# Kernel tuning notes

Hardware: AMD Instinct MI355X
Metric: run time of the kernel (lower is better)

## Reference

```python
import jax, jax.numpy as jnp
import numpy as np
from functools import partial

NPOINT = 1024
RADIUS = 0.2
NSAMPLE = 32
IN_CH = 64
MLP = [64, 64, 128]
EPS = 1e-5
B, N = 8, 4096


def setup_inputs() -> dict:
    key = jax.random.key(0)
    ks = jax.random.split(key, 2 + 2 * len(MLP))
    inp = {
        "xyz": jax.random.uniform(ks[0], (B, N, 3), jnp.float32),
        "points": jax.random.normal(ks[1], (B, N, IN_CH), jnp.float32),
    }
    last = IN_CH + 3
    for i, out in enumerate(MLP):
        # Conv2d 1x1 weight (out, in), kaiming-ish scale; BN gamma=1, beta=0
        inp[f"w{i}"] = jax.random.normal(ks[2 + 2 * i], (out, last), jnp.float32) / np.float32(np.sqrt(last))
        inp[f"b{i}"] = jnp.zeros((out,), jnp.float32)
        inp[f"g{i}"] = jnp.ones((out,), jnp.float32)
        inp[f"bt{i}"] = jnp.zeros((out,), jnp.float32)
        last = out
    return inp


def farthest_point_sample(xyz, npoint):
    # xyz: (B,N,3) -> (B,npoint) int32. Deterministic start at index 0
    # (original torch code uses randint for the seed point).
    Bb, Nn, _ = xyz.shape

    def step(carry, _):
        distance, farthest = carry
        centroid = jnp.take_along_axis(xyz, farthest[:, None, None], axis=1)  # (B,1,3)
        dist = jnp.sum((xyz - centroid) ** 2, axis=-1)                         # (B,N)
        distance = jnp.minimum(distance, dist)
        nxt = jnp.argmax(distance, axis=-1).astype(jnp.int32)
        return (distance, nxt), farthest

    init = (jnp.full((Bb, Nn), 1e10, xyz.dtype), jnp.zeros((Bb,), jnp.int32))
    _, idx = jax.lax.scan(step, init, None, length=npoint)  # (npoint,B)
    return idx.T


def query_ball_point(radius, nsample, xyz, new_xyz):
    # xyz: (B,N,3), new_xyz: (B,S,3) -> (B,S,nsample) indices into N
    Nn = xyz.shape[1]
    # (B,S,N) squared distances -- the big memory-bound intermediate
    sqrdists = jnp.sum((new_xyz[:, :, None, :] - xyz[:, None, :, :]) ** 2, axis=-1)
    group_idx = jnp.where(sqrdists > radius ** 2, Nn, jnp.arange(Nn, dtype=jnp.int32))
    group_idx = jnp.sort(group_idx, axis=-1)[:, :, :nsample]
    first = group_idx[:, :, :1]
    return jnp.where(group_idx == Nn, first, group_idx)


def _gather(p, i):
    # p: (N,C), i: (...,) -> (..., C)
    return p[i]


index_points = jax.vmap(_gather)  # batched over B


def reference(xyz, points, w0, b0, g0, bt0, w1, b1, g1, bt1, w2, b2, g2, bt2):
    fps_idx = farthest_point_sample(xyz, NPOINT)                # (B,S)
    new_xyz = index_points(xyz, fps_idx)                        # (B,S,3)
    group_idx = query_ball_point(RADIUS, NSAMPLE, xyz, new_xyz)  # (B,S,K)
    grouped_xyz = index_points(xyz, group_idx) - new_xyz[:, :, None, :]  # (B,S,K,3)
    grouped_pts = index_points(points, group_idx)               # (B,S,K,D)
    x = jnp.concatenate([grouped_xyz, grouped_pts], axis=-1)    # (B,S,K,3+D)

    for w, b, g, bt in ((w0, b0, g0, bt0), (w1, b1, g1, bt1), (w2, b2, g2, bt2)):
        x = jnp.einsum('bskc,oc->bsko', x, w) + b               # 1x1 conv
        mu = jnp.mean(x, axis=(0, 1, 2))                        # BN (training-mode batch stats)
        var = jnp.var(x, axis=(0, 1, 2))
        x = jax.nn.relu(g * (x - mu) * jax.lax.rsqrt(var + EPS) + bt)

    new_points = jnp.max(x, axis=2)                             # max over neighbors K -> (B,S,C')
    return new_xyz, new_points
```

## Files before the change

### kernel.cpp

```cpp
#include <hip/hip_runtime.h>
#include <cmath>

#define NB 8
#define NPTS 4096
#define NPT 1024
#define NSAMP 32
#define MTOT (NB*NPT*NSAMP)
#define NBLK 4096

typedef float v2f __attribute__((ext_vector_type(2)));

__global__ __launch_bounds__(512) void fps_kernel(const float* __restrict__ xyz,
                                                  float* __restrict__ new_xyz) {
#pragma clang fp contract(off)
  const int b = blockIdx.x;
  const int t = threadIdx.x;
  const int wv = t >> 6;
  const int lane = t & 63;
  __shared__ float4 sxyz[NPTS];
  __shared__ float4 sout[NPT];
  __shared__ unsigned long long skey[2][8];
  const float* X = xyz + (size_t)b * NPTS * 3;
  v2f px[4], py[4], pz[4], dist[4];
#pragma unroll
  for (int i = 0; i < 4; ++i) {
    int p0 = (2 * i) * 512 + t;
    int p1 = (2 * i + 1) * 512 + t;
    float x0 = X[p0 * 3 + 0], y0 = X[p0 * 3 + 1], z0 = X[p0 * 3 + 2];
    float x1 = X[p1 * 3 + 0], y1 = X[p1 * 3 + 1], z1 = X[p1 * 3 + 2];
    px[i] = (v2f){x0, x1}; py[i] = (v2f){y0, y1}; pz[i] = (v2f){z0, z1};
    sxyz[p0] = make_float4(x0, y0, z0, 0.0f);
    sxyz[p1] = make_float4(x1, y1, z1, 0.0f);
    dist[i] = (v2f){1e10f, 1e10f};
  }
  __syncthreads();
  float ccx = X[0], ccy = X[1], ccz = X[2];
  for (int s = 0; s < NPT; ++s) {
    if (t == 0) sout[s] = make_float4(ccx, ccy, ccz, 0.0f);
    v2f cx = (v2f){ccx, ccx}, cy = (v2f){ccy, ccy}, cz = (v2f){ccz, ccz};
    v2f nd[4];
#pragma unroll
    for (int i = 0; i < 4; ++i) {
      v2f dx = px[i] - cx;
      v2f dy = py[i] - cy;
      v2f dz = pz[i] - cz;
      v2f d = (dx * dx + dy * dy) + dz * dz;
      v2f m = __builtin_elementwise_min(dist[i], d);
      dist[i] = m;
      nd[i] = m;
    }
    v2f t01 = __builtin_elementwise_max(nd[0], nd[1]);
    v2f t23 = __builtin_elementwise_max(nd[2], nd[3]);
    v2f t03 = __builtin_elementwise_max(t01, t23);
    float lmax = fmaxf(t03.x, t03.y);
    unsigned km = __float_as_uint(lmax);
    {
      unsigned o;
      o = (unsigned)__builtin_amdgcn_update_dpp(0, (int)km, 0x111, 0xf, 0xf, false);
      km = o > km ? o : km;
      o = (unsigned)__builtin_amdgcn_update_dpp(0, (int)km, 0x112, 0xf, 0xf, false);
      km = o > km ? o : km;
      o = (unsigned)__builtin_amdgcn_update_dpp(0, (int)km, 0x114, 0xf, 0xf, false);
      km = o > km ? o : km;
      o = (unsigned)__builtin_amdgcn_update_dpp(0, (int)km, 0x118, 0xf, 0xf, false);
      km = o > km ? o : km;
      o = (unsigned)__builtin_amdgcn_update_dpp(0, (int)km, 0x142, 0xf, 0xf, false);
      km = o > km ? o : km;
      o = (unsigned)__builtin_amdgcn_update_dpp(0, (int)km, 0x143, 0xf, 0xf, false);
      km = o > km ? o : km;
    }
    unsigned wmax = (unsigned)__builtin_amdgcn_readlane((int)km, 63);
    unsigned long long m0 = __ballot(__float_as_uint(nd[0].x) == wmax);
    unsigned long long m1 = __ballot(__float_as_uint(nd[0].y) == wmax);
    unsigned long long m2 = __ballot(__float_as_uint(nd[1].x) == wmax);
    unsigned long long m3 = __ballot(__float_as_uint(nd[1].y) == wmax);
    unsigned long long m4 = __ballot(__float_as_uint(nd[2].x) == wmax);
    unsigned long long m5 = __ballot(__float_as_uint(nd[2].y) == wmax);
    unsigned long long m6 = __ballot(__float_as_uint(nd[3].x) == wmax);
    unsigned long long m7 = __ballot(__float_as_uint(nd[3].y) == wmax);
    unsigned long long mk = m7; int ord = 7;
    if (m6) { mk = m6; ord = 6; }
    if (m5) { mk = m5; ord = 5; }
    if (m4) { mk = m4; ord = 4; }
    if (m3) { mk = m3; ord = 3; }
    if (m2) { mk = m2; ord = 2; }
    if (m1) { mk = m1; ord = 1; }
    if (m0) { mk = m0; ord = 0; }
    int wlane = (int)__builtin_ctzll(mk);
    int idx = ord * 512 + wv * 64 + wlane;
    unsigned long long key = ((unsigned long long)wmax << 32)
                           | (unsigned int)(~idx);
    int par = s & 1;
    if (lane == 0) skey[par][wv] = key;
    __syncthreads();
    const ulonglong2* sk = (const ulonglong2*)skey[par];
    ulonglong2 A = sk[0], B = sk[1], C = sk[2], D = sk[3];
    unsigned long long a = A.x > A.y ? A.x : A.y;
    unsigned long long bq = B.x > B.y ? B.x : B.y;
    unsigned long long c = C.x > C.y ? C.x : C.y;
    unsigned long long dq = D.x > D.y ? D.x : D.y;
    unsigned long long ab = a > bq ? a : bq;
    unsigned long long cd = c > dq ? c : dq;
    unsigned long long kf = ab > cd ? ab : cd;
    int far = (int)(~(unsigned int)kf) & (NPTS - 1);
    float4 cc = sxyz[far];
    ccx = cc.x; ccy = cc.y; ccz = cc.z;
  }
  __syncthreads();
  float* outp = new_xyz + (size_t)b * NPT * 3;
  for (int j = t; j < NPT; j += 512) {
    float4 c = sout[j];
    outp[3 * j + 0] = c.x; outp[3 * j + 1] = c.y; outp[3 * j + 2] = c.z;
  }
}

__global__ __launch_bounds__(256) void ballq_kernel(const float* __restrict__ xyz,
                                                    const float* __restrict__ new_xyz,
                                                    int* __restrict__ gidx) {
  int w = (blockIdx.x * 256 + threadIdx.x) >> 6;
  int lane = threadIdx.x & 63;
  int b = w >> 10;
  const float* X = xyz + (size_t)b * NPTS * 3;
  float cx = new_xyz[w * 3 + 0], cy = new_xyz[w * 3 + 1], cz = new_xyz[w * 3 + 2];
  int* out = gidx + (size_t)w * NSAMP;
  int cnt = 0, first = -1;
  for (int c = 0; c < NPTS / 64; ++c) {
    int p = c * 64 + lane;
    float dx = __fsub_rn(X[p * 3 + 0], cx);
    float dy = __fsub_rn(X[p * 3 + 1], cy);
    float dz = __fsub_rn(X[p * 3 + 2], cz);
    float d = __fadd_rn(__fadd_rn(__fmul_rn(dx, dx), __fmul_rn(dy, dy)), __fmul_rn(dz, dz));
    bool inr = !(d > 0.04f);
    unsigned long long mask = __ballot(inr);
    if (mask) {
      if (first < 0) first = c * 64 + (int)__builtin_ctzll(mask);
      if (inr) {
        int pos = cnt + (int)__builtin_popcountll(mask & ((1ull << lane) - 1ull));
        if (pos < NSAMP) out[pos] = p;
      }
      cnt += (int)__builtin_popcountll(mask);
      if (cnt >= NSAMP) break;
    }
  }
  if (lane >= cnt && lane < NSAMP) out[lane] = first;
}

__global__ __launch_bounds__(256) void mlp_gemm_gather(
    const float* __restrict__ xyz, const float* __restrict__ points,
    const float* __restrict__ new_xyz, const int* __restrict__ gidx,
    const float* __restrict__ Wg, const float* __restrict__ bias,
    float* __restrict__ Yg, float* __restrict__ partials) {
  constexpr int O = 64, OJ = 4, KP4 = 17;
  __shared__ __align__(16) float sX[64 * 68];
  __shared__ __align__(16) float sWt[68 * O];
  const int t = threadIdx.x;
  const int m0 = blockIdx.x * 64;

  for (int i = t; i < O * 68; i += 256) {
    int k = i >> 6, o = i & 63;
    float w;
    if (k < 64) w = Wg[o * 67 + k + 3];
    else if (k < 67) w = Wg[o * 67 + (k - 64)];
    else w = 0.0f;
    sWt[k * O + o] = w;
  }
  {
    int r = t >> 2, q = t & 3;
    int m = m0 + r;
    int idx = gidx[m];
    int b = m >> 15;
    const float* prow = points + ((size_t)b * NPTS + idx) * 64;
#pragma unroll
    for (int c4 = q; c4 < 16; c4 += 4)
      *(float4*)&sX[r * 68 + 4 * c4] = *(const float4*)(prow + 4 * c4);
    if (q == 0) {
      int g = m >> 5;
      const float* xr = xyz + ((size_t)b * NPTS + idx) * 3;
      sX[r * 68 + 64] = __fsub_rn(xr[0], new_xyz[g * 3 + 0]);
      sX[r * 68 + 65] = __fsub_rn(xr[1], new_xyz[g * 3 + 1]);
      sX[r * 68 + 66] = __fsub_rn(xr[2], new_xyz[g * 3 + 2]);
      sX[r * 68 + 67] = 0.0f;
    }
  }
  __syncthreads();

  const int to = t & 15, tm = t >> 4;
  float acc[4][OJ];
#pragma unroll
  for (int i = 0; i < 4; ++i)
#pragma unroll
    for (int j = 0; j < OJ; ++j) acc[i][j] = 0.0f;

#pragma unroll
  for (int k4 = 0; k4 < KP4; ++k4) {
    float xs[4][4];
#pragma unroll
    for (int i = 0; i < 4; ++i) {
      float4 v = *(const float4*)&sX[(4 * tm + i) * 68 + 4 * k4];
      xs[i][0] = v.x; xs[i][1] = v.y; xs[i][2] = v.z; xs[i][3] = v.w;
    }
#pragma unroll
    for (int kk = 0; kk < 4; ++kk) {
      float4 wq = *(const float4*)&sWt[(4 * k4 + kk) * O + OJ * to];
      float wv[4] = {wq.x, wq.y, wq.z, wq.w};
#pragma unroll
      for (int i = 0; i < 4; ++i) {
        float xv = xs[i][kk];
#pragma unroll
        for (int j = 0; j < OJ; ++j) acc[i][j] = fmaf(xv, wv[j], acc[i][j]);
      }
    }
  }
#pragma unroll
  for (int j = 0; j < OJ; ++j) {
    float bb = bias[OJ * to + j];
#pragma unroll
    for (int i = 0; i < 4; ++i) acc[i][j] += bb;
  }
  float ps[OJ], ss[OJ];
#pragma unroll
  for (int j = 0; j < OJ; ++j) {
    ps[j] = ((acc[0][j] + acc[1][j]) + (acc[2][j] + acc[3][j]));
    ss[j] = ((acc[0][j] * acc[0][j] + acc[1][j] * acc[1][j]) +
             (acc[2][j] * acc[2][j] + acc[3][j] * acc[3][j]));
  }
  __syncthreads();
#pragma unroll
  for (int j = 0; j < OJ; ++j) {
    int o = OJ * to + j;
    sX[tm * O + o] = ps[j];
    sX[16 * O + tm * O + o] = ss[j];
  }
  __syncthreads();
  if (t < O) {
    float s1 = 0.0f, s2 = 0.0f;
#pragma unroll
    for (int r2 = 0; r2 < 16; ++r2) { s1 += sX[r2 * O + t]; s2 += sX[16 * O + r2 * O + t]; }
    partials[(size_t)t * NBLK + blockIdx.x] = s1;
    partials[(size_t)(O + t) * NBLK + blockIdx.x] = s2;
  }
#pragma unroll
  for (int i = 0; i < 4; ++i)
    *(float4*)&Yg[(size_t)(m0 + 4 * tm + i) * O + OJ * to] =
        make_float4(acc[i][0], acc[i][1], acc[i][2], acc[i][3]);
}

template<int O, bool WRITE_Y, bool DO_MM>
__global__ __launch_bounds__(256) void mlp_gemm(const float* __restrict__ Xg,
                                                const float* __restrict__ Wg,
                                                const float* __restrict__ bias,
                                                const float* __restrict__ ad,
                                                float* __restrict__ Yg,
                                                float* __restrict__ partials,
                                                float* __restrict__ mm) {
  constexpr int KDIM = 64, KP4 = 16;
  constexpr int OJ = O / 16;
  __shared__ __align__(16) float sX[64 * 68];
  __shared__ __align__(16) float sWt[KDIM * O];
  const int t = threadIdx.x;
  const int m0 = blockIdx.x * 64;

  for (int i = t; i < O * KDIM; i += 256) {
    int k = i / O;
    int o = i - k * O;
    sWt[k * O + o] = Wg[o * KDIM + k];
  }
  {
    int r = t >> 2, q = t & 3;
    const float* src = Xg + (size_t)(m0 + r) * KDIM;
    for (int c4 = q; c4 < KP4; c4 += 4) {
      float4 v = *(const float4*)(src + 4 * c4);
      float4 a = *(const float4*)(ad + 4 * c4);
      float4 d = *(const float4*)(ad + 128 + 4 * c4);
      v.x = fmaxf(fmaf(a.x, v.x, d.x), 0.0f);
      v.y = fmaxf(fmaf(a.y, v.y, d.y), 0.0f);
      v.z = fmaxf(fmaf(a.z, v.z, d.z), 0.0f);
      v.w = fmaxf(fmaf(a.w, v.w, d.w), 0.0f);
      *(float4*)&sX[r * 68 + 4 * c4] = v;
    }
  }
  __syncthreads();

  const int to = t & 15, tm = t >> 4;
  float acc[4][OJ];
#pragma unroll
  for (int i = 0; i < 4; ++i)
#pragma unroll
    for (int j = 0; j < OJ; ++j) acc[i][j] = 0.0f;

#pragma unroll
  for (int k4 = 0; k4 < KP4; ++k4) {
    float xs[4][4];
#pragma unroll
    for (int i = 0; i < 4; ++i) {
      float4 v = *(const float4*)&sX[(4 * tm + i) * 68 + 4 * k4];
      xs[i][0] = v.x; xs[i][1] = v.y; xs[i][2] = v.z; xs[i][3] = v.w;
    }
#pragma unroll
    for (int kk = 0; kk < 4; ++kk) {
      float wv[OJ];
#pragma unroll
      for (int j4 = 0; j4 < OJ / 4; ++j4) {
        float4 wq = *(const float4*)&sWt[(4 * k4 + kk) * O + OJ * to + 4 * j4];
        wv[4 * j4 + 0] = wq.x; wv[4 * j4 + 1] = wq.y;
        wv[4 * j4 + 2] = wq.z; wv[4 * j4 + 3] = wq.w;
      }
#pragma unroll
      for (int i = 0; i < 4; ++i) {
        float xv = xs[i][kk];
#pragma unroll
        for (int j = 0; j < OJ; ++j) acc[i][j] = fmaf(xv, wv[j], acc[i][j]);
      }
    }
  }
#pragma unroll
  for (int j = 0; j < OJ; ++j) {
    float bb = bias[OJ * to + j];
#pragma unroll
    for (int i = 0; i < 4; ++i) acc[i][j] += bb;
  }
  float ps[OJ], ss[OJ];
#pragma unroll
  for (int j = 0; j < OJ; ++j) {
    ps[j] = ((acc[0][j] + acc[1][j]) + (acc[2][j] + acc[3][j]));
    ss[j] = ((acc[0][j] * acc[0][j] + acc[1][j] * acc[1][j]) +
             (acc[2][j] * acc[2][j] + acc[3][j] * acc[3][j]));
  }
  __syncthreads();
#pragma unroll
  for (int j = 0; j < OJ; ++j) {
    int o = OJ * to + j;
    sX[tm * O + o] = ps[j];
    sX[16 * O + tm * O + o] = ss[j];
  }
  __syncthreads();
  if (t < O) {
    float s1 = 0.0f, s2 = 0.0f;
#pragma unroll
    for (int r2 = 0; r2 < 16; ++r2) { s1 += sX[r2 * O + t]; s2 += sX[16 * O + r2 * O + t]; }
    partials[(size_t)t * NBLK + blockIdx.x] = s1;
    partials[(size_t)(O + t) * NBLK + blockIdx.x] = s2;
  }
  if constexpr (WRITE_Y) {
#pragma unroll
    for (int i = 0; i < 4; ++i) {
#pragma unroll
      for (int j4 = 0; j4 < OJ / 4; ++j4) {
        *(float4*)&Yg[(size_t)(m0 + 4 * tm + i) * O + OJ * to + 4 * j4] =
            make_float4(acc[i][4 * j4 + 0], acc[i][4 * j4 + 1],
                        acc[i][4 * j4 + 2], acc[i][4 * j4 + 3]);
      }
    }
  }
  if constexpr (DO_MM) {
    float vmx[OJ], vmn[OJ];
#pragma unroll
    for (int j = 0; j < OJ; ++j) {
      vmx[j] = fmaxf(fmaxf(acc[0][j], acc[1][j]), fmaxf(acc[2][j], acc[3][j]));
      vmn[j] = fminf(fminf(acc[0][j], acc[1][j]), fminf(acc[2][j], acc[3][j]));
    }
    __syncthreads();
#pragma unroll
    for (int j = 0; j < OJ; ++j) {
      int o = OJ * to + j;
      sX[tm * O + o] = vmx[j];
      sX[16 * O + tm * O + o] = vmn[j];
    }
    __syncthreads();
    int g = t >> 7, o = t & 127;
    float mx = sX[(g * 8) * O + o];
    float mn = sX[16 * O + (g * 8) * O + o];
#pragma unroll
    for (int r2 = 1; r2 < 8; ++r2) {
      mx = fmaxf(mx, sX[(g * 8 + r2) * O + o]);
      mn = fminf(mn, sX[16 * O + (g * 8 + r2) * O + o]);
    }
    int row = (m0 >> 5) + g;
    mm[(size_t)row * O + o] = mx;
    mm[(size_t)8192 * O + (size_t)row * O + o] = mn;
  }
}

__global__ __launch_bounds__(256) void bn_finalize(const float* __restrict__ partials,
                                                   const float* __restrict__ g,
                                                   const float* __restrict__ bt,
                                                   float* __restrict__ ad, int O) {
  int o = blockIdx.x, t = threadIdx.x;
  const float* p1 = partials + (size_t)o * NBLK;
  const float* p2 = partials + (size_t)(O + o) * NBLK;
  float s1 = 0.0f, s2 = 0.0f;
  for (int i = t; i < NBLK; i += 256) { s1 += p1[i]; s2 += p2[i]; }
  __shared__ float r1[4], r2[4];
#pragma unroll
  for (int off = 32; off >= 1; off >>= 1) {
    s1 += __shfl_down(s1, off, 64);
    s2 += __shfl_down(s2, off, 64);
  }
  if ((t & 63) == 0) { r1[t >> 6] = s1; r2[t >> 6] = s2; }
  __syncthreads();
  if (t == 0) {
    float S1 = (r1[0] + r1[1]) + (r1[2] + r1[3]);
    float S2 = (r2[0] + r2[1]) + (r2[2] + r2[3]);
    const float invM = 1.0f / (float)MTOT;
    float mu = S1 * invM;
    float var = S2 * invM - mu * mu;
    float rs = 1.0f / sqrtf(var + 1e-5f);
    float a = g[o] * rs;
    ad[o] = a;
    ad[128 + o] = bt[o] - mu * a;
  }
}

__global__ __launch_bounds__(256) void final_kernel(const float* __restrict__ mm,
                                                    const float* __restrict__ ad,
                                                    float* __restrict__ out) {
  int gid = blockIdx.x * 256 + threadIdx.x;
  int o = gid & 127;
  float a = ad[o], d = ad[128 + o];
  float y = (a >= 0.0f) ? mm[gid] : mm[8192 * 128 + gid];
  out[gid] = fmaxf(fmaf(a, y, d), 0.0f);
}

extern "C" void kernel_launch(void* const* d_in, const int* in_sizes, int n_in,
                              void* d_out, int out_size, void* d_ws, size_t ws_size,
                              hipStream_t stream) {
  (void)in_sizes; (void)n_in; (void)out_size; (void)ws_size;
  const float* xyz    = (const float*)d_in[0];
  const float* points = (const float*)d_in[1];
  const float* w0  = (const float*)d_in[2];
  const float* b0  = (const float*)d_in[3];
  const float* g0  = (const float*)d_in[4];
  const float* bt0 = (const float*)d_in[5];
  const float* w1  = (const float*)d_in[6];
  const float* b1  = (const float*)d_in[7];
  const float* g1  = (const float*)d_in[8];
  const float* bt1 = (const float*)d_in[9];
  const float* w2  = (const float*)d_in[10];
  const float* b2  = (const float*)d_in[11];
  const float* g2  = (const float*)d_in[12];
  const float* bt2 = (const float*)d_in[13];

  float* out      = (float*)d_out;
  float* new_xyz  = out;
  float* out_pts  = out + 24576;

  float* wsf  = (float*)d_ws;
  int*   gidx = (int*)d_ws;
  float* Y2   = wsf + 262144;
  float* Y1   = Y2 + (size_t)MTOT * 68;
  float* part = Y1 + (size_t)MTOT * 64;
  float* ad1  = part + 2 * 128 * NBLK;
  float* ad2  = ad1 + 256;
  float* ad3  = ad2 + 256;
  float* mm   = ad3 + 256;

  fps_kernel<<<NB, 512, 0, stream>>>(xyz, new_xyz);
  ballq_kernel<<<(NB * NPT * 64) / 256, 256, 0, stream>>>(xyz, new_xyz, gidx);

  mlp_gemm_gather<<<NBLK, 256, 0, stream>>>(xyz, points, new_xyz, gidx,
                                            w0, b0, Y1, part);
  bn_finalize<<<64, 256, 0, stream>>>(part, g0, bt0, ad1, 64);

  mlp_gemm<64, true, false><<<NBLK, 256, 0, stream>>>(
      Y1, w1, b1, ad1, Y2, part, nullptr);
  bn_finalize<<<64, 256, 0, stream>>>(part, g1, bt1, ad2, 64);

  mlp_gemm<128, false, true><<<NBLK, 256, 0, stream>>>(
      Y2, w2, b2, ad2, nullptr, part, mm);
  bn_finalize<<<128, 256, 0, stream>>>(part, g2, bt2, ad3, 128);

  final_kernel<<<(8192 * 128) / 256, 256, 0, stream>>>(mm, ad3, out_pts);
}
```

Baseline: 920.0 us.

## Replace FP32 SIMT MLP GEMMs with FP16 MFMA matrix-core kernels

The three 1x1-conv GEMM kernels now run on 16x16x32 f16 MFMA instructions instead of scalar FP32 FMAs. Activations are packed to half precision when staged into shared memory, and a new prep kernel pre-transposes and converts the weights to padded fp16 layouts. The BN partial-sum and min/max reductions are reworked around the MFMA output layout using wave shuffles. This trades FP32 inputs for fp16 ones, which may hurt accuracy in the batch-norm statistics.

New measurement: 794.0 us. -13.7%, faster.

```diff
diff --git a/kernel.cpp b/kernel.cpp
--- a/kernel.cpp
+++ b/kernel.cpp
@@ -9,6 +9,41 @@
 #define NBLK 4096
 
 typedef float v2f __attribute__((ext_vector_type(2)));
+typedef _Float16 half8 __attribute__((ext_vector_type(8)));
+typedef float f32x4 __attribute__((ext_vector_type(4)));
+
+__device__ __forceinline__ unsigned int pk2h(float a, float b) {
+  _Float16 ha = (_Float16)a, hb = (_Float16)b;
+  unsigned short ua = __builtin_bit_cast(unsigned short, ha);
+  unsigned short ub = __builtin_bit_cast(unsigned short, hb);
+  return (unsigned int)ua | ((unsigned int)ub << 16);
+}
+__device__ __forceinline__ unsigned short f2h(float v) {
+  _Float16 h = (_Float16)v;
+  return __builtin_bit_cast(unsigned short, h);
+}
+
+__global__ __launch_bounds__(256) void prep_weights(
+    const float* __restrict__ w0, const float* __restrict__ w1,
+    const float* __restrict__ w2, unsigned short* __restrict__ Wt1,
+    unsigned short* __restrict__ Wt2, unsigned short* __restrict__ Wt3) {
+  int i = blockIdx.x * 256 + threadIdx.x;
+  if (i < 64 * 104) {
+    int o = i / 104, k = i - o * 104;
+    float v = 0.0f;
+    if (k < 64) v = w0[o * 67 + k + 3];
+    else if (k < 67) v = w0[o * 67 + (k - 64)];
+    Wt1[i] = f2h(v);
+  } else if (i < 64 * 104 + 64 * 72) {
+    int j = i - 64 * 104;
+    int o = j / 72, k = j - o * 72;
+    Wt2[j] = (k < 64) ? f2h(w1[o * 64 + k]) : (unsigned short)0;
+  } else if (i < 64 * 104 + 64 * 72 + 128 * 72) {
+    int l = i - 64 * 104 - 64 * 72;
+    int o = l / 72, k = l - o * 72;
+    Wt3[l] = (k < 64) ? f2h(w2[o * 64 + k]) : (unsigned short)0;
+  }
+}
 
 __global__ __launch_bounds__(512) void fps_kernel(const float* __restrict__ xyz,
                                                   float* __restrict__ new_xyz) {
@@ -145,239 +180,171 @@
   if (lane >= cnt && lane < NSAMP) out[lane] = first;
 }
 
-__global__ __launch_bounds__(256) void mlp_gemm_gather(
-    const float* __restrict__ xyz, const float* __restrict__ points,
-    const float* __restrict__ new_xyz, const int* __restrict__ gidx,
-    const float* __restrict__ Wg, const float* __restrict__ bias,
-    float* __restrict__ Yg, float* __restrict__ partials) {
-  constexpr int O = 64, OJ = 4, KP4 = 17;
-  __shared__ __align__(16) float sX[64 * 68];
-  __shared__ __align__(16) float sWt[68 * O];
+template<int KB, int KS, int O, bool GATHER, bool NORM_IN, bool WRITE_Y, bool DO_MM>
+__global__ __launch_bounds__(256) void mfma_gemm(
+    const float* __restrict__ Xg, const float* __restrict__ xyz,
+    const float* __restrict__ points, const float* __restrict__ new_xyz,
+    const int* __restrict__ gidx, const unsigned short* __restrict__ Wt,
+    const float* __restrict__ bias, const float* __restrict__ ad,
+    float* __restrict__ Yg, float* __restrict__ partials,
+    float* __restrict__ mm_out) {
+  constexpr int NT = O / 16;
+  __shared__ __align__(16) unsigned short sA[64 * KS];
+  __shared__ __align__(16) unsigned short sB[O * KS];
   const int t = threadIdx.x;
+  const int wv = t >> 6, lane = t & 63;
+  const int ml = lane & 15, qd = lane >> 4;
   const int m0 = blockIdx.x * 64;
 
-  for (int i = t; i < O * 68; i += 256) {
-    int k = i >> 6, o = i & 63;
-    float w;
-    if (k < 64) w = Wg[o * 67 + k + 3];
-    else if (k < 67) w = Wg[o * 67 + (k - 64)];
-    else w = 0.0f;
-    sWt[k * O + o] = w;
-  }
   {
+    const uint4* src = (const uint4*)Wt;
+    uint4* dst = (uint4*)sB;
+    constexpr int NB4 = O * KS / 8;
+    for (int i = t; i < NB4; i += 256) dst[i] = src[i];
+  }
+  if constexpr (GATHER) {
     int r = t >> 2, q = t & 3;
     int m = m0 + r;
     int idx = gidx[m];
     int b = m >> 15;
     const float* prow = points + ((size_t)b * NPTS + idx) * 64;
-#pragma unroll
-    for (int c4 = q; c4 < 16; c4 += 4)
-      *(float4*)&sX[r * 68 + 4 * c4] = *(const float4*)(prow + 4 * c4);
-    if (q == 0) {
+    unsigned int pk[12];
+    if (q < 2) {
+#pragma unroll
+      for (int j = 0; j < 6; ++j) {
+        float4 v = *(const float4*)(prow + q * 24 + 4 * j);
+        pk[2 * j] = pk2h(v.x, v.y);
+        pk[2 * j + 1] = pk2h(v.z, v.w);
+      }
+    } else if (q == 2) {
+#pragma unroll
+      for (int j = 0; j < 4; ++j) {
+        float4 v = *(const float4*)(prow + 48 + 4 * j);
+        pk[2 * j] = pk2h(v.x, v.y);
+        pk[2 * j + 1] = pk2h(v.z, v.w);
+      }
       int g = m >> 5;
       const float* xr = xyz + ((size_t)b * NPTS + idx) * 3;
-      sX[r * 68 + 64] = __fsub_rn(xr[0], new_xyz[g * 3 + 0]);
-      sX[r * 68 + 65] = __fsub_rn(xr[1], new_xyz[g * 3 + 1]);
-      sX[r * 68 + 66] = __fsub_rn(xr[2], new_xyz[g * 3 + 2]);
-      sX[r * 68 + 67] = 0.0f;
-    }
-  }
-  __syncthreads();
-
-  const int to = t & 15, tm = t >> 4;
-  float acc[4][OJ];
-#pragma unroll
-  for (int i = 0; i < 4; ++i)
-#pragma unroll
-    for (int j = 0; j < OJ; ++j) acc[i][j] = 0.0f;
-
-#pragma unroll
-  for (int k4 = 0; k4 < KP4; ++k4) {
-    float xs[4][4];
-#pragma unroll
-    for (int i = 0; i < 4; ++i) {
-      float4 v = *(const float4*)&sX[(4 * tm + i) * 68 + 4 * k4];
-      xs[i][0] = v.x; xs[i][1] = v.y; xs[i][2] = v.z; xs[i][3] = v.w;
-    }
-#pragma unroll
-    for (int kk = 0; kk < 4; ++kk) {
-      float4 wq = *(const float4*)&sWt[(4 * k4 + kk) * O + OJ * to];
-      float wv[4] = {wq.x, wq.y, wq.z, wq.w};
-#pragma unroll
-      for (int i = 0; i < 4; ++i) {
-        float xv = xs[i][kk];
-#pragma unroll
-        for (int j = 0; j < OJ; ++j) acc[i][j] = fmaf(xv, wv[j], acc[i][j]);
+      float dx = __fsub_rn(xr[0], new_xyz[g * 3 + 0]);
+      float dy = __fsub_rn(xr[1], new_xyz[g * 3 + 1]);
+      float dz = __fsub_rn(xr[2], new_xyz[g * 3 + 2]);
+      pk[8] = pk2h(dx, dy);
+      pk[9] = pk2h(dz, 0.0f);
+      pk[10] = 0; pk[11] = 0;
+    } else {
+#pragma unroll
+      for (int j = 0; j < 12; ++j) pk[j] = 0;
+    }
+    uint4* dst = (uint4*)&sA[r * KS + q * 24];
+    dst[0] = make_uint4(pk[0], pk[1], pk[2], pk[3]);
+    dst[1] = make_uint4(pk[4], pk[5], pk[6], pk[7]);
+    dst[2] = make_uint4(pk[8], pk[9], pk[10], pk[11]);
+  } else {
+    int r = t >> 2, q = t & 3;
+    const float* src = Xg + (size_t)(m0 + r) * 64 + q * 16;
+    unsigned int pk[8];
+#pragma unroll
+    for (int j = 0; j < 4; ++j) {
+      float4 v = *(const float4*)(src + 4 * j);
+      if constexpr (NORM_IN) {
+        float4 a = *(const float4*)(ad + q * 16 + 4 * j);
+        float4 d = *(const float4*)(ad + 128 + q * 16 + 4 * j);
+        v.x = fmaxf(fmaf(a.x, v.x, d.x), 0.0f);
+        v.y = fmaxf(fmaf(a.y, v.y, d.y), 0.0f);
+        v.z = fmaxf(fmaf(a.z, v.z, d.z), 0.0f);
+        v.w = fmaxf(fmaf(a.w, v.w, d.w), 0.0f);
       }
-    }
-  }
-#pragma unroll
-  for (int j = 0; j < OJ; ++j) {
-    float bb = bias[OJ * to + j];
-#pragma unroll
-    for (int i = 0; i < 4; ++i) acc[i][j] += bb;
-  }
-  float ps[OJ], ss[OJ];
-#pragma unroll
-  for (int j = 0; j < OJ; ++j) {
-    ps[j] = ((acc[0][j] + acc[1][j]) + (acc[2][j] + acc[3][j]));
-    ss[j] = ((acc[0][j] * acc[0][j] + acc[1][j] * acc[1][j]) +
-             (acc[2][j] * acc[2][j] + acc[3][j] * acc[3][j]));
-  }
-  __syncthreads();
-#pragma unroll
-  for (int j = 0; j < OJ; ++j) {
-    int o = OJ * to + j;
-    sX[tm * O + o] = ps[j];
-    sX[16 * O + tm * O + o] = ss[j];
+      pk[2 * j] = pk2h(v.x, v.y);
+      pk[2 * j + 1] = pk2h(v.z, v.w);
+    }
+    uint4* dst = (uint4*)&sA[r * KS + q * 16];
+    dst[0] = make_uint4(pk[0], pk[1], pk[2], pk[3]);
+    dst[1] = make_uint4(pk[4], pk[5], pk[6], pk[7]);
+  }
+  __syncthreads();
+
+  f32x4 acc[NT];
+#pragma unroll
+  for (int nt = 0; nt < NT; ++nt) acc[nt] = f32x4{0.0f, 0.0f, 0.0f, 0.0f};
+
+#pragma unroll
+  for (int kb = 0; kb < KB; ++kb) {
+    int kof = kb * 32 + qd * 8;
+    uint4 au = *(const uint4*)&sA[(16 * wv + ml) * KS + kof];
+    half8 af = __builtin_bit_cast(half8, au);
+#pragma unroll
+    for (int nt = 0; nt < NT; ++nt) {
+      uint4 bu = *(const uint4*)&sB[(nt * 16 + ml) * KS + kof];
+      half8 bf = __builtin_bit_cast(half8, bu);
+      acc[nt] = __builtin_amdgcn_mfma_f32_16x16x32_f16(af, bf, acc[nt], 0, 0, 0);
+    }
+  }
+#pragma unroll
+  for (int nt = 0; nt < NT; ++nt) {
+    float bb = bias[nt * 16 + ml];
+    acc[nt][0] += bb; acc[nt][1] += bb; acc[nt][2] += bb; acc[nt][3] += bb;
+  }
+  float s1[NT], s2[NT];
+#pragma unroll
+  for (int nt = 0; nt < NT; ++nt) {
+    f32x4 a4 = acc[nt];
+    s1[nt] = (a4[0] + a4[1]) + (a4[2] + a4[3]);
+    s2[nt] = (a4[0] * a4[0] + a4[1] * a4[1]) + (a4[2] * a4[2] + a4[3] * a4[3]);
+    s1[nt] += __shfl_down(s1[nt], 32, 64);
+    s1[nt] += __shfl_down(s1[nt], 16, 64);
+    s2[nt] += __shfl_down(s2[nt], 32, 64);
+    s2[nt] += __shfl_down(s2[nt], 16, 64);
+  }
+  if constexpr (WRITE_Y) {
+#pragma unroll
+    for (int nt = 0; nt < NT; ++nt)
+#pragma unroll
+      for (int r = 0; r < 4; ++r)
+        Yg[(size_t)(m0 + 16 * wv + qd * 4 + r) * O + nt * 16 + ml] = acc[nt][r];
+  }
+  float mx[NT], mn[NT];
+  if constexpr (DO_MM) {
+#pragma unroll
+    for (int nt = 0; nt < NT; ++nt) {
+      f32x4 a4 = acc[nt];
+      mx[nt] = fmaxf(fmaxf(a4[0], a4[1]), fmaxf(a4[2], a4[3]));
+      mn[nt] = fminf(fminf(a4[0], a4[1]), fminf(a4[2], a4[3]));
+      mx[nt] = fmaxf(mx[nt], __shfl_down(mx[nt], 32, 64));
+      mx[nt] = fmaxf(mx[nt], __shfl_down(mx[nt], 16, 64));
+      mn[nt] = fminf(mn[nt], __shfl_down(mn[nt], 32, 64));
+      mn[nt] = fminf(mn[nt], __shfl_down(mn[nt], 16, 64));
+    }
+  }
+  __syncthreads();
+  float* scr = (float*)sA;
+  if (qd == 0) {
+#pragma unroll
+    for (int nt = 0; nt < NT; ++nt) {
+      scr[wv * O + nt * 16 + ml] = s1[nt];
+      scr[4 * O + wv * O + nt * 16 + ml] = s2[nt];
+    }
+    if constexpr (DO_MM) {
+#pragma unroll
+      for (int nt = 0; nt < NT; ++nt) {
+        scr[8 * O + wv * O + nt * 16 + ml] = mx[nt];
+        scr[12 * O + wv * O + nt * 16 + ml] = mn[nt];
+      }
+    }
   }
   __syncthreads();
   if (t < O) {
-    float s1 = 0.0f, s2 = 0.0f;
-#pragma unroll
-    for (int r2 = 0; r2 < 16; ++r2) { s1 += sX[r2 * O + t]; s2 += sX[16 * O + r2 * O + t]; }
-    partials[(size_t)t * NBLK + blockIdx.x] = s1;
-    partials[(size_t)(O + t) * NBLK + blockIdx.x] = s2;
-  }
-#pragma unroll
-  for (int i = 0; i < 4; ++i)
-    *(float4*)&Yg[(size_t)(m0 + 4 * tm + i) * O + OJ * to] =
-        make_float4(acc[i][0], acc[i][1], acc[i][2], acc[i][3]);
-}
-
-template<int O, bool WRITE_Y, bool DO_MM>
-__global__ __launch_bounds__(256) void mlp_gemm(const float* __restrict__ Xg,
-                                                const float* __restrict__ Wg,
-                                                const float* __restrict__ bias,
-                                                const float* __restrict__ ad,
-                                                float* __restrict__ Yg,
-                                                float* __restrict__ partials,
-                                                float* __restrict__ mm) {
-  constexpr int KDIM = 64, KP4 = 16;
-  constexpr int OJ = O / 16;
-  __shared__ __align__(16) float sX[64 * 68];
-  __shared__ __align__(16) float sWt[KDIM * O];
-  const int t = threadIdx.x;
-  const int m0 = blockIdx.x * 64;
-
-  for (int i = t; i < O * KDIM; i += 256) {
-    int k = i / O;
-    int o = i - k * O;
-    sWt[k * O + o] = Wg[o * KDIM + k];
-  }
-  {
-    int r = t >> 2, q = t & 3;
-    const float* src = Xg + (size_t)(m0 + r) * KDIM;
-    for (int c4 = q; c4 < KP4; c4 += 4) {
-      float4 v = *(const float4*)(src + 4 * c4);
-      float4 a = *(const float4*)(ad + 4 * c4);
-      float4 d = *(const float4*)(ad + 128 + 4 * c4);
-      v.x = fmaxf(fmaf(a.x, v.x, d.x), 0.0f);
-      v.y = fmaxf(fmaf(a.y, v.y, d.y), 0.0f);
-      v.z = fmaxf(fmaf(a.z, v.z, d.z), 0.0f);
-      v.w = fmaxf(fmaf(a.w, v.w, d.w), 0.0f);
-      *(float4*)&sX[r * 68 + 4 * c4] = v;
-    }
-  }
-  __syncthreads();
-
-  const int to = t & 15, tm = t >> 4;
-  float acc[4][OJ];
-#pragma unroll
-  for (int i = 0; i < 4; ++i)
-#pragma unroll
-    for (int j = 0; j < OJ; ++j) acc[i][j] = 0.0f;
-
-#pragma unroll
-  for (int k4 = 0; k4 < KP4; ++k4) {
-    float xs[4][4];
-#pragma unroll
-    for (int i = 0; i < 4; ++i) {
-      float4 v = *(const float4*)&sX[(4 * tm + i) * 68 + 4 * k4];
-      xs[i][0] = v.x; xs[i][1] = v.y; xs[i][2] = v.z; xs[i][3] = v.w;
-    }
-#pragma unroll
-    for (int kk = 0; kk < 4; ++kk) {
-      float wv[OJ];
-#pragma unroll
-      for (int j4 = 0; j4 < OJ / 4; ++j4) {
-        float4 wq = *(const float4*)&sWt[(4 * k4 + kk) * O + OJ * to + 4 * j4];
-        wv[4 * j4 + 0] = wq.x; wv[4 * j4 + 1] = wq.y;
-        wv[4 * j4 + 2] = wq.z; wv[4 * j4 + 3] = wq.w;
-      }
-#pragma unroll
-      for (int i = 0; i < 4; ++i) {
-        float xv = xs[i][kk];
-#pragma unroll
-        for (int j = 0; j < OJ; ++j) acc[i][j] = fmaf(xv, wv[j], acc[i][j]);
-      }
-    }
-  }
-#pragma unroll
-  for (int j = 0; j < OJ; ++j) {
-    float bb = bias[OJ * to + j];
-#pragma unroll
-    for (int i = 0; i < 4; ++i) acc[i][j] += bb;
-  }
-  float ps[OJ], ss[OJ];
-#pragma unroll
-  for (int j = 0; j < OJ; ++j) {
-    ps[j] = ((acc[0][j] + acc[1][j]) + (acc[2][j] + acc[3][j]));
-    ss[j] = ((acc[0][j] * acc[0][j] + acc[1][j] * acc[1][j]) +
-             (acc[2][j] * acc[2][j] + acc[3][j] * acc[3][j]));
-  }
-  __syncthreads();
-#pragma unroll
-  for (int j = 0; j < OJ; ++j) {
-    int o = OJ * to + j;
-    sX[tm * O + o] = ps[j];
-    sX[16 * O + tm * O + o] = ss[j];
-  }
-  __syncthreads();
-  if (t < O) {
-    float s1 = 0.0f, s2 = 0.0f;
-#pragma unroll
-    for (int r2 = 0; r2 < 16; ++r2) { s1 += sX[r2 * O + t]; s2 += sX[16 * O + r2 * O + t]; }
-    partials[(size_t)t * NBLK + blockIdx.x] = s1;
-    partials[(size_t)(O + t) * NBLK + blockIdx.x] = s2;
-  }
-  if constexpr (WRITE_Y) {
-#pragma unroll
-    for (int i = 0; i < 4; ++i) {
-#pragma unroll
-      for (int j4 = 0; j4 < OJ / 4; ++j4) {
-        *(float4*)&Yg[(size_t)(m0 + 4 * tm + i) * O + OJ * to + 4 * j4] =
-            make_float4(acc[i][4 * j4 + 0], acc[i][4 * j4 + 1],
-                        acc[i][4 * j4 + 2], acc[i][4 * j4 + 3]);
-      }
-    }
+    float a = (scr[t] + scr[O + t]) + (scr[2 * O + t] + scr[3 * O + t]);
+    float b2 = (scr[4 * O + t] + scr[5 * O + t]) + (scr[6 * O + t] + scr[7 * O + t]);
+    partials[(size_t)t * NBLK + blockIdx.x] = a;
+    partials[(size_t)(O + t) * NBLK + blockIdx.x] = b2;
   }
   if constexpr (DO_MM) {
-    float vmx[OJ], vmn[OJ];
-#pragma unroll
-    for (int j = 0; j < OJ; ++j) {
-      vmx[j] = fmaxf(fmaxf(acc[0][j], acc[1][j]), fmaxf(acc[2][j], acc[3][j]));
-      vmn[j] = fminf(fminf(acc[0][j], acc[1][j]), fminf(acc[2][j], acc[3][j]));
-    }
-    __syncthreads();
-#pragma unroll
-    for (int j = 0; j < OJ; ++j) {
-      int o = OJ * to + j;
-      sX[tm * O + o] = vmx[j];
-      sX[16 * O + tm * O + o] = vmn[j];
-    }
-    __syncthreads();
-    int g = t >> 7, o = t & 127;
-    float mx = sX[(g * 8) * O + o];
-    float mn = sX[16 * O + (g * 8) * O + o];
-#pragma unroll
-    for (int r2 = 1; r2 < 8; ++r2) {
-      mx = fmaxf(mx, sX[(g * 8 + r2) * O + o]);
-      mn = fminf(mn, sX[16 * O + (g * 8 + r2) * O + o]);
-    }
+    int o = t & 127, g = t >> 7;
+    float gmx = fmaxf(scr[8 * O + (2 * g) * O + o], scr[8 * O + (2 * g + 1) * O + o]);
+    float gmn = fminf(scr[12 * O + (2 * g) * O + o], scr[12 * O + (2 * g + 1) * O + o]);
     int row = (m0 >> 5) + g;
-    mm[(size_t)row * O + o] = mx;
-    mm[(size_t)8192 * O + (size_t)row * O + o] = mn;
+    mm_out[(size_t)row * O + o] = gmx;
+    mm_out[(size_t)8192 * O + (size_t)row * O + o] = gmn;
   }
 }
 
@@ -453,20 +420,24 @@
   float* ad2  = ad1 + 256;
   float* ad3  = ad2 + 256;
   float* mm   = ad3 + 256;
-
+  unsigned short* Wt1 = (unsigned short*)(mm + 2 * 8192 * 128);
+  unsigned short* Wt2 = Wt1 + 64 * 104;
+  unsigned short* Wt3 = Wt2 + 64 * 72;
+
+  prep_weights<<<80, 256, 0, stream>>>(w0, w1, w2, Wt1, Wt2, Wt3);
   fps_kernel<<<NB, 512, 0, stream>>>(xyz, new_xyz);
   ballq_kernel<<<(NB * NPT * 64) / 256, 256, 0, stream>>>(xyz, new_xyz, gidx);
 
-  mlp_gemm_gather<<<NBLK, 256, 0, stream>>>(xyz, points, new_xyz, gidx,
-                                            w0, b0, Y1, part);
+  mfma_gemm<3, 104, 64, true, false, true, false><<<NBLK, 256, 0, stream>>>(
+      nullptr, xyz, points, new_xyz, gidx, Wt1, b0, nullptr, Y1, part, nullptr);
   bn_finalize<<<64, 256, 0, stream>>>(part, g0, bt0, ad1, 64);
 
-  mlp_gemm<64, true, false><<<NBLK, 256, 0, stream>>>(
-      Y1, w1, b1, ad1, Y2, part, nullptr);
+  mfma_gemm<2, 72, 64, false, true, true, false><<<NBLK, 256, 0, stream>>>(
+      Y1, nullptr, nullptr, nullptr, nullptr, Wt2, b1, ad1, Y2, part, nullptr);
   bn_finalize<<<64, 256, 0, stream>>>(part, g1, bt1, ad2, 64);
 
-  mlp_gemm<128, false, true><<<NBLK, 256, 0, stream>>>(
-      Y2, w2, b2, ad2, nullptr, part, mm);
+  mfma_gemm<2, 72, 128, false, true, false, true><<<NBLK, 256, 0, stream>>>(
+      Y2, nullptr, nullptr, nullptr, nullptr, Wt3, b2, ad2, nullptr, part, mm);
   bn_finalize<<<128, 256, 0, stream>>>(part, g2, bt2, ad3, 128);
 
   final_kernel<<<(8192 * 128) / 256, 256, 0, stream>>>(mm, ad3, out_pts);
```
